# Kernel tuning notes

Hardware: AMD Instinct MI355X
Metric: run time of the kernel (lower is better)

Reference implementation:

```python
import jax, jax.numpy as jnp
import numpy as np

NUM_GROUPS = 32
EPS = 1e-6


def group_norm(x, gamma, beta):
    # x: [B, C, H, W]
    B, C, H, W = x.shape
    xg = x.reshape(B, NUM_GROUPS, C // NUM_GROUPS, H, W)
    mean = jnp.mean(xg, axis=(2, 3, 4), keepdims=True)
    var = jnp.var(xg, axis=(2, 3, 4), keepdims=True)
    xn = (xg - mean) * jax.lax.rsqrt(var + EPS)
    xn = xn.reshape(B, C, H, W)
    return xn * gamma[None, :, None, None] + beta[None, :, None, None]


def conv1x1(x, w, b):
    # x: [B, C, H, W], w: [Cout, Cin], b: [Cout]
    return jnp.einsum('bchw,dc->bdhw', x, w) + b[None, :, None, None]


def setup_inputs() -> dict:
    key = jax.random.key(0)
    ks = jax.random.split(key, 11)
    B, C, H, W = 4, 512, 64, 64
    s = 1.0 / np.sqrt(C)
    return {
        'x': jax.random.normal(ks[0], (B, C, H, W), dtype=jnp.float32),
        'gn_gamma': jnp.ones((C,), dtype=jnp.float32),
        'gn_beta': jnp.zeros((C,), dtype=jnp.float32),
        'wq': jax.random.normal(ks[1], (C, C), dtype=jnp.float32) * s,
        'bq': jax.random.normal(ks[2], (C,), dtype=jnp.float32) * 0.01,
        'wk': jax.random.normal(ks[3], (C, C), dtype=jnp.float32) * s,
        'bk': jax.random.normal(ks[4], (C,), dtype=jnp.float32) * 0.01,
        'wv': jax.random.normal(ks[5], (C, C), dtype=jnp.float32) * s,
        'bv': jax.random.normal(ks[6], (C,), dtype=jnp.float32) * 0.01,
        'wo': jax.random.normal(ks[7], (C, C), dtype=jnp.float32) * s,
        'bo': jax.random.normal(ks[8], (C,), dtype=jnp.float32) * 0.01,
    }


def reference(x, gn_gamma, gn_beta, wq, bq, wk, bk, wv, bv, wo, bo):
    B, C, H, W = x.shape
    h = group_norm(x, gn_gamma, gn_beta)
    q = conv1x1(h, wq, bq).reshape(B, C, H * W)  # [B, C, N]
    k = conv1x1(h, wk, bk).reshape(B, C, H * W)
    v = conv1x1(h, wv, bv).reshape(B, C, H * W)
    scale = jnp.asarray(C, x.dtype) ** -0.5
    # scores[b, i, j] = q_i . k_j
    scores = jnp.einsum('bci,bcj->bij', q, k) * scale  # [B, N, N]
    attn = jax.nn.softmax(scores, axis=2)
    # out[b, c, i] = sum_j v[b, c, j] * attn[b, i, j]
    out = jnp.einsum('bcj,bij->bci', v, attn).reshape(B, C, H, W)
    out = conv1x1(out, wo, bo)
    return x + out
```

## Files before the change

### kernel.cpp

```cpp
#include <hip/hip_runtime.h>

using uint = unsigned int;
typedef short bf16x8 __attribute__((ext_vector_type(8)));
typedef _Float16 f16x8 __attribute__((ext_vector_type(8)));
typedef float f32x4 __attribute__((ext_vector_type(4)));
typedef int i32x4 __attribute__((ext_vector_type(4)));
typedef int i32x8 __attribute__((ext_vector_type(8)));

static constexpr int Cc = 512;
static constexpr int Nn = 4096;
static constexpr size_t NC = (size_t)Nn * Cc;
static constexpr size_t SN = (size_t)Nn * Nn;

__device__ __forceinline__ unsigned short f2bf(float f) {
    unsigned int u = __builtin_bit_cast(unsigned int, f);
    u = (u + 0x7fff + ((u >> 16) & 1)) >> 16;
    return (unsigned short)u;
}
__device__ __forceinline__ unsigned short f2h(float f) {
    _Float16 h = (_Float16)f;
    return __builtin_bit_cast(unsigned short, h);
}

__device__ __forceinline__ void gll16(const void* g, void* l) {
    __builtin_amdgcn_global_load_lds(
        (const __attribute__((address_space(1))) void*)g,
        (__attribute__((address_space(3))) void*)l, 16, 0, 0);
}

__device__ __forceinline__ f32x4 mfma_fp8_k128(i32x8 a, i32x8 b, f32x4 c) {
    return __builtin_amdgcn_mfma_scale_f32_16x16x128_f8f6f4(
        a, b, c, 0 , 0 , 0, 0x7F7F7F7F, 0, 0x7F7F7F7F);
}

__global__ void cvt_kernel(const float* __restrict__ in, unsigned short* __restrict__ out, int n4) {
    int i = blockIdx.x * blockDim.x + threadIdx.x;
    if (i < n4) {
        float4 v = ((const float4*)in)[i];
        out[i * 4 + 0] = f2bf(v.x);
        out[i * 4 + 1] = f2bf(v.y);
        out[i * 4 + 2] = f2bf(v.z);
        out[i * 4 + 3] = f2bf(v.w);
    }
}

__global__ void zero_kernel(float* __restrict__ p, int n4) {
    int i = blockIdx.x * blockDim.x + threadIdx.x;
    if (i < n4) ((float4*)p)[i] = make_float4(0.f, 0.f, 0.f, 0.f);
}

__global__ void gn_stats_kernel(const float* __restrict__ x, float* __restrict__ meanb,
                                float* __restrict__ rsb) {
    int bg = blockIdx.x;
    const float* slab = x + (size_t)bg * 16 * Nn;
    const float4* s4 = (const float4*)slab;
    int t = threadIdx.x;
    float s1 = 0.f, s2 = 0.f;
#pragma unroll 8
    for (int k = 0; k < 64; ++k) {
        float4 v = s4[k * 256 + t];
        s1 += v.x + v.y + v.z + v.w;
        s2 += v.x * v.x + v.y * v.y + v.z * v.z + v.w * v.w;
    }
#pragma unroll
    for (int o = 32; o > 0; o >>= 1) { s1 += __shfl_down(s1, o); s2 += __shfl_down(s2, o); }
    __shared__ float r1[4], r2[4];
    int wv_ = t >> 6, ln = t & 63;
    if (ln == 0) { r1[wv_] = s1; r2[wv_] = s2; }
    __syncthreads();
    if (t == 0) {
        float a1 = r1[0] + r1[1] + r1[2] + r1[3];
        float a2 = r2[0] + r2[1] + r2[2] + r2[3];
        float mean = a1 * (1.f / 65536.f);
        float var = a2 * (1.f / 65536.f) - mean * mean;
        meanb[bg] = mean;
        rsb[bg] = rsqrtf(var + 1e-6f);
    }
}

__global__ __launch_bounds__(256) void gn_norm_kernel(
    const float* __restrict__ x, const float* __restrict__ meanb, const float* __restrict__ rsb,
    const float* __restrict__ gamma, const float* __restrict__ beta,
    unsigned short* __restrict__ h_t) {
    __shared__ float tile[64][65];
    int n0 = blockIdx.x * 64, c0 = blockIdx.y * 64, b = blockIdx.z;
    int t = threadIdx.x;
    const float* xb = x + (size_t)b * Cc * Nn;
#pragma unroll
    for (int j = 0; j < 4; ++j) {
        int i = j * 256 + t;
        int c = i >> 4;
        int n4 = i & 15;
        int cg = c0 + c;
        float4 v = ((const float4*)(xb + (size_t)cg * Nn + n0))[n4];
        int g = cg >> 4;
        float mean = meanb[b * 32 + g], rs = rsb[b * 32 + g];
        float ga = gamma[cg] * rs;
        float be = beta[cg] - mean * ga;
        tile[n4 * 4 + 0][c] = v.x * ga + be;
        tile[n4 * 4 + 1][c] = v.y * ga + be;
        tile[n4 * 4 + 2][c] = v.z * ga + be;
        tile[n4 * 4 + 3][c] = v.w * ga + be;
    }
    __syncthreads();
    int n = t >> 2;
    int cpart = (t & 3) * 16;
    unsigned short o[16];
#pragma unroll
    for (int q = 0; q < 16; ++q) o[q] = f2bf(tile[n][cpart + q]);
    unsigned short* dst = h_t + (size_t)b * NC + (size_t)(n0 + n) * Cc + c0 + cpart;
    ((uint4*)dst)[0] = ((uint4*)o)[0];
    ((uint4*)dst)[1] = ((uint4*)o)[1];
}

template <int BM, int DT, int BIAS_MODE, int OUT_MODE, int HAS_RES>
__global__ __launch_bounds__(256, 2) void gemm_bt(
    const unsigned short* __restrict__ A, int lda, size_t sA,
    const unsigned short* __restrict__ Bt, int ldb, size_t sB,
    void* __restrict__ outp, int ldc, size_t sC,
    const float* __restrict__ bias,
    const float* __restrict__ res, size_t sR,
    int K, float alpha) {
    constexpr int MT = BM / 32;
    __shared__ unsigned short lA[BM * 64];
    __shared__ unsigned short lB[128 * 64];
    int z = blockIdx.z;
    A += (size_t)z * sA;
    Bt += (size_t)z * sB;
    int m0 = blockIdx.y * BM, n0 = blockIdx.x * 128;
    int t = threadIdx.x;
    int lane = t & 63, wave = t >> 6;
    int wm = wave >> 1, wn = wave & 1;
    int lo = lane & 15, quad = lane >> 4;

    f32x4 acc[MT][4];
#pragma unroll
    for (int a1 = 0; a1 < MT; ++a1)
#pragma unroll
        for (int a2 = 0; a2 < 4; ++a2) acc[a1][a2] = (f32x4){0.f, 0.f, 0.f, 0.f};

    for (int k0 = 0; k0 < K; k0 += 64) {
#pragma unroll
        for (int p = 0; p < MT; ++p) {
            int ci = p * 256 + t;
            int row = ci >> 3;
            int gs = (ci ^ row) & 7;
            gll16(A + (size_t)(m0 + row) * lda + k0 + gs * 8, &lA[(size_t)ci * 8]);
        }
#pragma unroll
        for (int p = 0; p < 4; ++p) {
            int ci = p * 256 + t;
            int row = ci >> 3;
            int gs = (ci ^ row) & 7;
            gll16(Bt + (size_t)(n0 + row) * ldb + k0 + gs * 8, &lB[(size_t)ci * 8]);
        }
        __syncthreads();
#pragma unroll
        for (int ks = 0; ks < 2; ++ks) {
            int G = quad + ks * 4;
            bf16x8 af[MT], bfr[4];
#pragma unroll
            for (int mt = 0; mt < MT; ++mt) {
                int R = wm * (BM / 2) + mt * 16 + lo;
                af[mt] = *(const bf16x8*)&lA[R * 64 + (((G ^ R) & 7) << 3)];
            }
#pragma unroll
            for (int nt = 0; nt < 4; ++nt) {
                int R = wn * 64 + nt * 16 + lo;
                bfr[nt] = *(const bf16x8*)&lB[R * 64 + (((G ^ R) & 7) << 3)];
            }
#pragma unroll
            for (int mt = 0; mt < MT; ++mt)
#pragma unroll
                for (int nt = 0; nt < 4; ++nt) {
                    if (DT == 0)
                        acc[mt][nt] = __builtin_amdgcn_mfma_f32_16x16x32_bf16(af[mt], bfr[nt], acc[mt][nt], 0, 0, 0);
                    else
                        acc[mt][nt] = __builtin_amdgcn_mfma_f32_16x16x32_f16(
                            __builtin_bit_cast(f16x8, af[mt]), __builtin_bit_cast(f16x8, bfr[nt]),
                            acc[mt][nt], 0, 0, 0);
                }
        }
        __syncthreads();
    }

    size_t zc = (size_t)z * sC;
    float* outf = (float*)outp + zc;
    unsigned short* outb = (unsigned short*)outp + zc;
    unsigned char* outc = (unsigned char*)outp + zc;
    const float* resz = HAS_RES ? res + (size_t)z * sR : nullptr;

#pragma unroll
    for (int mt = 0; mt < MT; ++mt) {
#pragma unroll
        for (int nt = 0; nt < 4; ++nt) {
            int row = m0 + wm * (BM / 2) + mt * 16 + quad * 4;
            int col = n0 + wn * 64 + nt * 16 + lo;
            float bn = (BIAS_MODE == 2) ? bias[col] : 0.f;
#pragma unroll
            for (int r = 0; r < 4; ++r) {
                float vv = acc[mt][nt][r];
                if (BIAS_MODE == 1) vv += bias[row + r];
                if (BIAS_MODE == 2) vv += bn;
                vv *= alpha;
                if (OUT_MODE == 3) {
                    float e = fmaxf(fminf(vv, 448.f), -448.f);
                    int pk = __builtin_amdgcn_cvt_pk_fp8_f32(e, e, 0, false);
                    outc[(size_t)(row + r) * ldc + col] = (unsigned char)(pk & 0xff);
                } else {
                    size_t off = (size_t)(row + r) * ldc + col;
                    if (HAS_RES) vv += resz[off];
                    if (OUT_MODE == 0) outf[off] = vv;
                    else if (OUT_MODE == 1) outb[off] = f2bf(vv);
                    else outb[off] = f2h(vv);
                }
            }
        }
    }
}

__global__ __launch_bounds__(256, 2) void qk_fp8(
    const unsigned char* __restrict__ Q, const unsigned char* __restrict__ Kt,
    unsigned char* __restrict__ S, float* __restrict__ lsum, float alpha) {
    __shared__ unsigned char lA[128 * 128];
    __shared__ unsigned char lB[128 * 128];
    int z = blockIdx.z;
    Q += (size_t)z * NC;
    Kt += (size_t)z * NC;
    S += (size_t)z * SN;
    lsum += (size_t)z * Nn;
    int m0 = blockIdx.y * 128, n0 = blockIdx.x * 128;
    int t = threadIdx.x;
    int lane = t & 63, wave = t >> 6;
    int wm = wave >> 1, wn = wave & 1;
    int lo = lane & 15, quad = lane >> 4;

    f32x4 acc[4][4];
#pragma unroll
    for (int a1 = 0; a1 < 4; ++a1)
#pragma unroll
        for (int a2 = 0; a2 < 4; ++a2) acc[a1][a2] = (f32x4){0.f, 0.f, 0.f, 0.f};

    for (int k0 = 0; k0 < Cc; k0 += 128) {
#pragma unroll
        for (int p = 0; p < 4; ++p) {
            int ci = p * 256 + t;
            int row = ci >> 3, g = ci & 7;
            int gs = g ^ (row & 7);
            gll16(Q + (size_t)(m0 + row) * Cc + k0 + gs * 16, &lA[ci * 16]);
        }
#pragma unroll
        for (int p = 0; p < 4; ++p) {
            int ci = p * 256 + t;
            int row = ci >> 3, g = ci & 7;
            int gs = g ^ (row & 7);
            gll16(Kt + (size_t)(n0 + row) * Cc + k0 + gs * 16, &lB[ci * 16]);
        }
        __syncthreads();
        int g0 = quad * 2;
        i32x8 bq8[4];
#pragma unroll
        for (int nt = 0; nt < 4; ++nt) {
            int R = wn * 64 + nt * 16 + lo;
            i32x4 b_lo = *(const i32x4*)&lB[R * 128 + ((g0 ^ (R & 7)) << 4)];
            i32x4 b_hi = *(const i32x4*)&lB[R * 128 + (((g0 + 1) ^ (R & 7)) << 4)];
            bq8[nt] = __builtin_shufflevector(b_lo, b_hi, 0, 1, 2, 3, 4, 5, 6, 7);
        }
#pragma unroll
        for (int mt = 0; mt < 4; ++mt) {
            int R = wm * 64 + mt * 16 + lo;
            i32x4 a_lo = *(const i32x4*)&lA[R * 128 + ((g0 ^ (R & 7)) << 4)];
            i32x4 a_hi = *(const i32x4*)&lA[R * 128 + (((g0 + 1) ^ (R & 7)) << 4)];
            i32x8 aq8 = __builtin_shufflevector(a_lo, a_hi, 0, 1, 2, 3, 4, 5, 6, 7);
#pragma unroll
            for (int nt = 0; nt < 4; ++nt)
                acc[mt][nt] = mfma_fp8_k128(aq8, bq8[nt], acc[mt][nt]);
        }
        __syncthreads();
    }

#pragma unroll
    for (int mt = 0; mt < 4; ++mt) {
        int row = m0 + wm * 64 + mt * 16 + quad * 4;
        float rsum[4] = {0.f, 0.f, 0.f, 0.f};
#pragma unroll
        for (int nt = 0; nt < 4; ++nt) {
            int col = n0 + wn * 64 + nt * 16 + lo;
#pragma unroll
            for (int r = 0; r < 4; ++r) {
                float e = __expf(acc[mt][nt][r] * alpha - 2.f);
                e = fminf(e, 448.f);
                int pk = __builtin_amdgcn_cvt_pk_fp8_f32(e, e, 0, false);
                S[(size_t)(row + r) * Nn + col] = (unsigned char)(pk & 0xff);
                rsum[r] += __builtin_amdgcn_cvt_f32_fp8(pk, 0);
            }
        }
#pragma unroll
        for (int o = 1; o < 16; o <<= 1) {
#pragma unroll
            for (int r = 0; r < 4; ++r) rsum[r] += __shfl_xor(rsum[r], o);
        }
        if (lo == 0) {
#pragma unroll
            for (int r = 0; r < 4; ++r) atomicAdd(&lsum[row + r], rsum[r]);
        }
    }
}

__global__ __launch_bounds__(256, 3) void pv_fp8(
    const unsigned char* __restrict__ S, const unsigned char* __restrict__ V,
    const float* __restrict__ lsum, unsigned short* __restrict__ o_t) {
    __shared__ unsigned char lA[128 * 128];
    __shared__ unsigned char lB[128 * 128];
    int z = blockIdx.z;
    S += (size_t)z * SN;
    V += (size_t)z * NC;
    lsum += (size_t)z * Nn;
    o_t += (size_t)z * NC;
    int m0 = blockIdx.y * 128, n0 = blockIdx.x * 128;
    int t = threadIdx.x;
    int lane = t & 63, wave = t >> 6;
    int wm = wave >> 1, wn = wave & 1;
    int lo = lane & 15, quad = lane >> 4;

    f32x4 acc[4][4];
#pragma unroll
    for (int a1 = 0; a1 < 4; ++a1)
#pragma unroll
        for (int a2 = 0; a2 < 4; ++a2) acc[a1][a2] = (f32x4){0.f, 0.f, 0.f, 0.f};

    for (int k0 = 0; k0 < Nn; k0 += 128) {
#pragma unroll
        for (int p = 0; p < 4; ++p) {
            int ci = p * 256 + t;
            int row = ci >> 3, g = ci & 7;
            int gs = g ^ (row & 7);
            gll16(S + (size_t)(m0 + row) * Nn + k0 + gs * 16, &lA[ci * 16]);
        }
#pragma unroll
        for (int p = 0; p < 4; ++p) {
            int ci = p * 256 + t;
            int row = ci >> 3, g = ci & 7;
            int gs = g ^ (row & 7);
            gll16(V + (size_t)(n0 + row) * Nn + k0 + gs * 16, &lB[ci * 16]);
        }
        __syncthreads();
        int g0 = quad * 2;
        i32x8 bq8[4];
#pragma unroll
        for (int nt = 0; nt < 4; ++nt) {
            int R = wn * 64 + nt * 16 + lo;
            i32x4 b_lo = *(const i32x4*)&lB[R * 128 + ((g0 ^ (R & 7)) << 4)];
            i32x4 b_hi = *(const i32x4*)&lB[R * 128 + (((g0 + 1) ^ (R & 7)) << 4)];
            bq8[nt] = __builtin_shufflevector(b_lo, b_hi, 0, 1, 2, 3, 4, 5, 6, 7);
        }
#pragma unroll
        for (int mt = 0; mt < 4; ++mt) {
            int R = wm * 64 + mt * 16 + lo;
            i32x4 a_lo = *(const i32x4*)&lA[R * 128 + ((g0 ^ (R & 7)) << 4)];
            i32x4 a_hi = *(const i32x4*)&lA[R * 128 + (((g0 + 1) ^ (R & 7)) << 4)];
            i32x8 aq8 = __builtin_shufflevector(a_lo, a_hi, 0, 1, 2, 3, 4, 5, 6, 7);
#pragma unroll
            for (int nt = 0; nt < 4; ++nt)
                acc[mt][nt] = mfma_fp8_k128(aq8, bq8[nt], acc[mt][nt]);
        }
        __syncthreads();
    }

#pragma unroll
    for (int mt = 0; mt < 4; ++mt)
#pragma unroll
        for (int nt = 0; nt < 4; ++nt) {
            int row = m0 + wm * 64 + mt * 16 + quad * 4;
            int col = n0 + wn * 64 + nt * 16 + lo;
#pragma unroll
            for (int r = 0; r < 4; ++r) {
                float vv = acc[mt][nt][r] / lsum[row + r];
                o_t[(size_t)(row + r) * Cc + col] = f2bf(vv);
            }
        }
}

extern "C" void kernel_launch(void* const* d_in, const int* in_sizes, int n_in,
                              void* d_out, int out_size, void* d_ws, size_t ws_size,
                              hipStream_t stream) {
    const float* x     = (const float*)d_in[0];
    const float* gamma = (const float*)d_in[1];
    const float* beta  = (const float*)d_in[2];
    const float* wq = (const float*)d_in[3];
    const float* bq = (const float*)d_in[4];
    const float* wk = (const float*)d_in[5];
    const float* bk = (const float*)d_in[6];
    const float* wv = (const float*)d_in[7];
    const float* bv = (const float*)d_in[8];
    const float* wo = (const float*)d_in[9];
    const float* bo = (const float*)d_in[10];

    char* ws = (char*)d_ws;
    unsigned short* h_t  = (unsigned short*)(ws);
    unsigned char*  q_8  = (unsigned char*)(ws + 16777216);
    unsigned char*  k_8  = (unsigned char*)(ws + 33554432);
    unsigned char*  v_8  = (unsigned char*)(ws + 50331648);
    unsigned short* o_t  = (unsigned short*)(ws + 67108864);
    unsigned char*  S    = (unsigned char*)(ws + 83886080);
    unsigned short* wqb  = (unsigned short*)(ws + 218103808);
    unsigned short* wkb  = (unsigned short*)(ws + 218628096);
    unsigned short* wvb  = (unsigned short*)(ws + 219152384);
    unsigned short* wob  = (unsigned short*)(ws + 219676672);
    float* statm         = (float*)(ws + 220200960);
    float* statr         = (float*)(ws + 220201984);
    float* lsum          = (float*)(ws + 220203008);

    const float SCALE = 0.044194173824159216f;

    cvt_kernel<<<256, 256, 0, stream>>>(wq, wqb, 65536);
    cvt_kernel<<<256, 256, 0, stream>>>(wk, wkb, 65536);
    cvt_kernel<<<256, 256, 0, stream>>>(wv, wvb, 65536);
    cvt_kernel<<<256, 256, 0, stream>>>(wo, wob, 65536);
    zero_kernel<<<16, 256, 0, stream>>>(lsum, 4096);

    gn_stats_kernel<<<128, 256, 0, stream>>>(x, statm, statr);
    gn_norm_kernel<<<dim3(64, 8, 4), 256, 0, stream>>>(x, statm, statr, gamma, beta, h_t);

    gemm_bt<128, 0, 2, 3, 0><<<dim3(4, 32, 4), 256, 0, stream>>>(
        h_t, Cc, NC, wqb, Cc, 0, q_8, Cc, NC, bq, nullptr, 0, Cc, 1.f);
    gemm_bt<128, 0, 2, 3, 0><<<dim3(4, 32, 4), 256, 0, stream>>>(
        h_t, Cc, NC, wkb, Cc, 0, k_8, Cc, NC, bk, nullptr, 0, Cc, 1.f);
    gemm_bt<128, 0, 1, 3, 0><<<dim3(32, 4, 4), 256, 0, stream>>>(
        wvb, Cc, 0, h_t, Cc, NC, v_8, Nn, NC, bv, nullptr, 0, Cc, 1.f);

    qk_fp8<<<dim3(32, 32, 4), 256, 0, stream>>>(q_8, k_8, S, lsum, SCALE);
    pv_fp8<<<dim3(4, 32, 4), 256, 0, stream>>>(S, v_8, lsum, o_t);

    gemm_bt<128, 0, 1, 0, 1><<<dim3(32, 4, 4), 256, 0, stream>>>(
        wob, Cc, 0, o_t, Cc, NC, d_out, Nn, NC, bo, x, NC, Cc, 1.f);
}
```

Baseline: 309.7 us.

## Swap MFMA operand order for row-contiguous packed stores in QK and PV

Result: faster. 302.6 us (-2.3%).

```diff
diff --git a/kernel.cpp b/kernel.cpp
--- a/kernel.cpp
+++ b/kernel.cpp
@@ -4,8 +4,11 @@
 typedef short bf16x8 __attribute__((ext_vector_type(8)));
 typedef _Float16 f16x8 __attribute__((ext_vector_type(8)));
 typedef float f32x4 __attribute__((ext_vector_type(4)));
-typedef int i32x4 __attribute__((ext_vector_type(4)));
+typedef long i64;
+typedef i64 i64x2 __attribute__((ext_vector_type(2)));
+typedef i64 i64x4 __attribute__((ext_vector_type(4)));
 typedef int i32x8 __attribute__((ext_vector_type(8)));
+typedef unsigned short u16x4 __attribute__((ext_vector_type(4)));
 
 static constexpr int Cc = 512;
 static constexpr int Nn = 4096;
@@ -31,6 +34,14 @@
 __device__ __forceinline__ f32x4 mfma_fp8_k128(i32x8 a, i32x8 b, f32x4 c) {
     return __builtin_amdgcn_mfma_scale_f32_16x16x128_f8f6f4(
         a, b, c, 0 , 0 , 0, 0x7F7F7F7F, 0, 0x7F7F7F7F);
+}
+
+__device__ __forceinline__ i32x8 ld_frag256(const unsigned char* base, int R, int g0) {
+    const unsigned char* p = base + R * 128;
+    i64x2 l0 = *(const i64x2*)(p + ((g0 ^ (R & 7)) << 4));
+    i64x2 l1 = *(const i64x2*)(p + (((g0 + 1) ^ (R & 7)) << 4));
+    i64x4 c4 = {l0[0], l0[1], l1[0], l1[1]};
+    return __builtin_bit_cast(i32x8, c4);
 }
 
 __global__ void cvt_kernel(const float* __restrict__ in, unsigned short* __restrict__ out, int n4) {
@@ -219,7 +230,7 @@
     }
 }
 
-__global__ __launch_bounds__(256, 2) void qk_fp8(
+__global__ __launch_bounds__(256, 3) void qk_fp8(
     const unsigned char* __restrict__ Q, const unsigned char* __restrict__ Kt,
     unsigned char* __restrict__ S, float* __restrict__ lsum, float alpha) {
     __shared__ unsigned char lA[128 * 128];
@@ -258,52 +269,46 @@
         }
         __syncthreads();
         int g0 = quad * 2;
-        i32x8 bq8[4];
-#pragma unroll
-        for (int nt = 0; nt < 4; ++nt) {
-            int R = wn * 64 + nt * 16 + lo;
-            i32x4 b_lo = *(const i32x4*)&lB[R * 128 + ((g0 ^ (R & 7)) << 4)];
-            i32x4 b_hi = *(const i32x4*)&lB[R * 128 + (((g0 + 1) ^ (R & 7)) << 4)];
-            bq8[nt] = __builtin_shufflevector(b_lo, b_hi, 0, 1, 2, 3, 4, 5, 6, 7);
-        }
-#pragma unroll
-        for (int mt = 0; mt < 4; ++mt) {
-            int R = wm * 64 + mt * 16 + lo;
-            i32x4 a_lo = *(const i32x4*)&lA[R * 128 + ((g0 ^ (R & 7)) << 4)];
-            i32x4 a_hi = *(const i32x4*)&lA[R * 128 + (((g0 + 1) ^ (R & 7)) << 4)];
-            i32x8 aq8 = __builtin_shufflevector(a_lo, a_hi, 0, 1, 2, 3, 4, 5, 6, 7);
-#pragma unroll
-            for (int nt = 0; nt < 4; ++nt)
-                acc[mt][nt] = mfma_fp8_k128(aq8, bq8[nt], acc[mt][nt]);
-        }
-        __syncthreads();
-    }
-
-#pragma unroll
-    for (int mt = 0; mt < 4; ++mt) {
-        int row = m0 + wm * 64 + mt * 16 + quad * 4;
-        float rsum[4] = {0.f, 0.f, 0.f, 0.f};
-#pragma unroll
-        for (int nt = 0; nt < 4; ++nt) {
-            int col = n0 + wn * 64 + nt * 16 + lo;
-#pragma unroll
-            for (int r = 0; r < 4; ++r) {
-                float e = __expf(acc[mt][nt][r] * alpha - 2.f);
-                e = fminf(e, 448.f);
-                int pk = __builtin_amdgcn_cvt_pk_fp8_f32(e, e, 0, false);
-                S[(size_t)(row + r) * Nn + col] = (unsigned char)(pk & 0xff);
-                rsum[r] += __builtin_amdgcn_cvt_f32_fp8(pk, 0);
-            }
-        }
-#pragma unroll
-        for (int o = 1; o < 16; o <<= 1) {
-#pragma unroll
-            for (int r = 0; r < 4; ++r) rsum[r] += __shfl_xor(rsum[r], o);
-        }
-        if (lo == 0) {
-#pragma unroll
-            for (int r = 0; r < 4; ++r) atomicAdd(&lsum[row + r], rsum[r]);
-        }
+        i32x8 qf[4];
+#pragma unroll
+        for (int qt = 0; qt < 4; ++qt) qf[qt] = ld_frag256(lA, wm * 64 + qt * 16 + lo, g0);
+#pragma unroll
+        for (int jt = 0; jt < 4; ++jt) {
+            i32x8 kf = ld_frag256(lB, wn * 64 + jt * 16 + lo, g0);
+#pragma unroll
+            for (int qt = 0; qt < 4; ++qt)
+                acc[jt][qt] = mfma_fp8_k128(kf, qf[qt], acc[jt][qt]);
+        }
+        __syncthreads();
+    }
+
+    float rs[4] = {0.f, 0.f, 0.f, 0.f};
+#pragma unroll
+    for (int jt = 0; jt < 4; ++jt) {
+        int j = n0 + wn * 64 + jt * 16 + quad * 4;
+#pragma unroll
+        for (int qt = 0; qt < 4; ++qt) {
+            int q = m0 + wm * 64 + qt * 16 + lo;
+            float e0 = fminf(__expf(acc[jt][qt][0] * alpha - 2.f), 448.f);
+            float e1 = fminf(__expf(acc[jt][qt][1] * alpha - 2.f), 448.f);
+            float e2 = fminf(__expf(acc[jt][qt][2] * alpha - 2.f), 448.f);
+            float e3 = fminf(__expf(acc[jt][qt][3] * alpha - 2.f), 448.f);
+            int d = __builtin_amdgcn_cvt_pk_fp8_f32(e0, e1, 0, false);
+            d = __builtin_amdgcn_cvt_pk_fp8_f32(e2, e3, d, true);
+            *(uint*)&S[(size_t)q * Nn + j] = (uint)d;
+            rs[qt] += __builtin_amdgcn_cvt_f32_fp8(d, 0) + __builtin_amdgcn_cvt_f32_fp8(d, 1) +
+                      __builtin_amdgcn_cvt_f32_fp8(d, 2) + __builtin_amdgcn_cvt_f32_fp8(d, 3);
+        }
+    }
+#pragma unroll
+    for (int qt = 0; qt < 4; ++qt) {
+        rs[qt] += __shfl_xor(rs[qt], 16);
+        rs[qt] += __shfl_xor(rs[qt], 32);
+    }
+    if (quad == 0) {
+#pragma unroll
+        for (int qt = 0; qt < 4; ++qt)
+            atomicAdd(&lsum[m0 + wm * 64 + qt * 16 + lo], rs[qt]);
     }
 }
 
@@ -346,39 +351,34 @@
         }
         __syncthreads();
         int g0 = quad * 2;
-        i32x8 bq8[4];
-#pragma unroll
-        for (int nt = 0; nt < 4; ++nt) {
-            int R = wn * 64 + nt * 16 + lo;
-            i32x4 b_lo = *(const i32x4*)&lB[R * 128 + ((g0 ^ (R & 7)) << 4)];
-            i32x4 b_hi = *(const i32x4*)&lB[R * 128 + (((g0 + 1) ^ (R & 7)) << 4)];
-            bq8[nt] = __builtin_shufflevector(b_lo, b_hi, 0, 1, 2, 3, 4, 5, 6, 7);
-        }
-#pragma unroll
-        for (int mt = 0; mt < 4; ++mt) {
-            int R = wm * 64 + mt * 16 + lo;
-            i32x4 a_lo = *(const i32x4*)&lA[R * 128 + ((g0 ^ (R & 7)) << 4)];
-            i32x4 a_hi = *(const i32x4*)&lA[R * 128 + (((g0 + 1) ^ (R & 7)) << 4)];
-            i32x8 aq8 = __builtin_shufflevector(a_lo, a_hi, 0, 1, 2, 3, 4, 5, 6, 7);
-#pragma unroll
-            for (int nt = 0; nt < 4; ++nt)
-                acc[mt][nt] = mfma_fp8_k128(aq8, bq8[nt], acc[mt][nt]);
-        }
-        __syncthreads();
-    }
-
-#pragma unroll
-    for (int mt = 0; mt < 4; ++mt)
-#pragma unroll
-        for (int nt = 0; nt < 4; ++nt) {
-            int row = m0 + wm * 64 + mt * 16 + quad * 4;
-            int col = n0 + wn * 64 + nt * 16 + lo;
-#pragma unroll
-            for (int r = 0; r < 4; ++r) {
-                float vv = acc[mt][nt][r] / lsum[row + r];
-                o_t[(size_t)(row + r) * Cc + col] = f2bf(vv);
-            }
-        }
+        i32x8 sf[4];
+#pragma unroll
+        for (int qt = 0; qt < 4; ++qt) sf[qt] = ld_frag256(lA, wm * 64 + qt * 16 + lo, g0);
+#pragma unroll
+        for (int ct = 0; ct < 4; ++ct) {
+            i32x8 vf = ld_frag256(lB, wn * 64 + ct * 16 + lo, g0);
+#pragma unroll
+            for (int qt = 0; qt < 4; ++qt)
+                acc[ct][qt] = mfma_fp8_k128(vf, sf[qt], acc[ct][qt]);
+        }
+        __syncthreads();
+    }
+
+#pragma unroll
+    for (int qt = 0; qt < 4; ++qt) {
+        int q = m0 + wm * 64 + qt * 16 + lo;
+        float inv = 1.f / lsum[q];
+#pragma unroll
+        for (int ct = 0; ct < 4; ++ct) {
+            int c = n0 + wn * 64 + ct * 16 + quad * 4;
+            u16x4 o;
+            o[0] = f2bf(acc[ct][qt][0] * inv);
+            o[1] = f2bf(acc[ct][qt][1] * inv);
+            o[2] = f2bf(acc[ct][qt][2] * inv);
+            o[3] = f2bf(acc[ct][qt][3] * inv);
+            *(u16x4*)&o_t[(size_t)q * Cc + c] = o;
+        }
+    }
 }
 
 extern "C" void kernel_launch(void* const* d_in, const int* in_sizes, int n_in,
```
